# Kernel tuning notes

Hardware: AMD Instinct MI355X
Metric: run time of the kernel (lower is better)

## Reference

```python
import jax, jax.numpy as jnp
import numpy as np

WIN = 7
K1, K2 = 0.01, 0.03
NP_ = WIN * WIN
COV_NORM = NP_ / (NP_ - 1)


def _box_conv(x, w):
    return jax.lax.conv_general_dilated(
        x, w, window_strides=(1, 1), padding='VALID',
        dimension_numbers=('NCHW', 'OIHW', 'NCHW'))


def setup_inputs() -> dict:
    key = jax.random.key(0)
    k1, k2 = jax.random.split(key)
    B, C, H, W = 64, 2, 320, 320
    X = jax.random.uniform(k1, (B, C, H, W), dtype=jnp.float32)
    Y = jax.random.uniform(k2, (B, C, H, W), dtype=jnp.float32)
    data_range = jnp.ones((B, 1, 1, 1), dtype=jnp.float32)
    w = jnp.ones((1, C, WIN, WIN), dtype=jnp.float32) / (WIN * WIN)
    return {"X": X, "Y": Y, "data_range": data_range, "w": w}


def reference(X, Y, data_range, w):
    C1 = (K1 * data_range) ** 2
    C2 = (K2 * data_range) ** 2
    ux = _box_conv(X, w)
    uy = _box_conv(Y, w)
    uxx = _box_conv(X * X, w)
    uyy = _box_conv(Y * Y, w)
    uxy = _box_conv(X * Y, w)
    vx = COV_NORM * (uxx - ux * ux)
    vy = COV_NORM * (uyy - uy * uy)
    vxy = COV_NORM * (uxy - ux * uy)
    A1 = 2 * ux * uy + C1
    A2 = 2 * vxy + C2
    B1 = ux ** 2 + uy ** 2 + C1
    B2 = vx + vy + C2
    S = (A1 * A2) / (B1 * B2)
    return 1 - S.mean()
```

## Files before the change

### kernel.cpp

```cpp
#include <hip/hip_runtime.h>

#define WW 320
#define OWID 314
#define OHEI 314
#define BB 64
#define RPB 28
#define NBAND 12
#define NSTRIP 79
#define NTH 256
#define NBLK ((BB * NBAND * NSTRIP) / NTH)

__device__ __forceinline__ void compute_h(
    const float* __restrict__ X0, const float* __restrict__ X1,
    const float* __restrict__ Y0, const float* __restrict__ Y1,
    int off, int o2, float* __restrict__ h)
{
    float4 ax0 = *(const float4*)(X0 + off);
    float4 ax1 = *(const float4*)(X0 + off + 4);
    float4 ax2 = *(const float4*)(X0 + off + o2);
    float4 bx0 = *(const float4*)(X1 + off);
    float4 bx1 = *(const float4*)(X1 + off + 4);
    float4 bx2 = *(const float4*)(X1 + off + o2);
    float4 ay0 = *(const float4*)(Y0 + off);
    float4 ay1 = *(const float4*)(Y0 + off + 4);
    float4 ay2 = *(const float4*)(Y0 + off + o2);
    float4 by0 = *(const float4*)(Y1 + off);
    float4 by1 = *(const float4*)(Y1 + off + 4);
    float4 by2 = *(const float4*)(Y1 + off + o2);

    float x0[10] = {ax0.x, ax0.y, ax0.z, ax0.w, ax1.x, ax1.y, ax1.z, ax1.w, ax2.x, ax2.y};
    float x1[10] = {bx0.x, bx0.y, bx0.z, bx0.w, bx1.x, bx1.y, bx1.z, bx1.w, bx2.x, bx2.y};
    float y0[10] = {ay0.x, ay0.y, ay0.z, ay0.w, ay1.x, ay1.y, ay1.z, ay1.w, ay2.x, ay2.y};
    float y1[10] = {by0.x, by0.y, by0.z, by0.w, by1.x, by1.y, by1.z, by1.w, by2.x, by2.y};

    float sx[10], sy[10], sxx[10], syy[10], sxy[10];
    #pragma unroll
    for (int j = 0; j < 10; ++j) {
        sx[j]  = x0[j] + x1[j];
        sy[j]  = y0[j] + y1[j];
        sxx[j] = x0[j] * x0[j] + x1[j] * x1[j];
        syy[j] = y0[j] * y0[j] + y1[j] * y1[j];
        sxy[j] = x0[j] * y0[j] + x1[j] * y1[j];
    }
    #pragma unroll
    for (int q = 0; q < 5; ++q) {
        const float* m = (q == 0) ? sx : (q == 1) ? sy : (q == 2) ? sxx : (q == 3) ? syy : sxy;
        float t0 = ((m[0] + m[1]) + (m[2] + m[3])) + ((m[4] + m[5]) + m[6]);
        float t1 = t0 - m[0] + m[7];
        float t2 = t1 - m[1] + m[8];
        float t3 = t2 - m[2] + m[9];
        h[q * 4 + 0] = t0; h[q * 4 + 1] = t1; h[q * 4 + 2] = t2; h[q * 4 + 3] = t3;
    }
}

__global__ __launch_bounds__(NTH, 1) void ssim_main(
    const float* __restrict__ X, const float* __restrict__ Y,
    const float* __restrict__ dr, double* __restrict__ acc,
    unsigned* __restrict__ counter, float* __restrict__ out)
{
    const int wi   = blockIdx.x * NTH + threadIdx.x;
    const int s    = wi % NSTRIP;
    const int g    = wi / NSTRIP;
    const int band = g % NBAND;
    const int b    = g / NBAND;
    const int r0   = band * RPB;
    const int cb   = s * 4;
    const int o2   = (cb <= 308) ? 8 : 4;

    const size_t plane = (size_t)WW * WW;
    const float* X0 = X + (size_t)b * 2 * plane;
    const float* X1 = X0 + plane;
    const float* Y0 = Y + (size_t)b * 2 * plane;
    const float* Y1 = Y0 + plane;

    const float d  = dr[b];
    const float C1 = (0.01f * d) * (0.01f * d);
    const float C2 = (0.03f * d) * (0.03f * d);

    float cm[4];
    #pragma unroll
    for (int j = 0; j < 4; ++j) cm[j] = (cb + j < OWID) ? 1.0f : 0.0f;

    float ring[7][20];
    float v[20];
    #pragma unroll
    for (int i = 0; i < 20; ++i) v[i] = 0.0f;

    #pragma unroll
    for (int k = 0; k < 6; ++k) {
        compute_h(X0, X1, Y0, Y1, (r0 + k) * WW + cb, o2, &ring[k][0]);
        #pragma unroll
        for (int i = 0; i < 20; ++i) v[i] += ring[k][i];
    }

    float ssum = 0.0f;
    for (int t7 = 0; t7 < RPB; t7 += 7) {
        #pragma unroll
        for (int k = 0; k < 7; ++k) {
            const int t    = r0 + t7 + k;
            const int rin  = min(t + 6, WW - 1);
            const int slot = (k + 6) % 7;

            compute_h(X0, X1, Y0, Y1, rin * WW + cb, o2, &ring[slot][0]);
            #pragma unroll
            for (int i = 0; i < 20; ++i) v[i] += ring[slot][i];

            if (t < OHEI) {
                const float inv = 1.0f / 49.0f;
                const float cn  = 49.0f / 48.0f;
                #pragma unroll
                for (int j = 0; j < 4; ++j) {
                    float ux  = v[j]      * inv, uy  = v[4 + j]  * inv;
                    float uxx = v[8 + j]  * inv, uyy = v[12 + j] * inv, uxy = v[16 + j] * inv;
                    float vx  = cn * (uxx - ux * ux);
                    float vy  = cn * (uyy - uy * uy);
                    float vxy = cn * (uxy - ux * uy);
                    float A1  = 2.0f * ux * uy + C1;
                    float A2  = 2.0f * vxy + C2;
                    float B1  = ux * ux + uy * uy + C1;
                    float B2  = vx + vy + C2;
                    ssum += cm[j] * (A1 * A2) / (B1 * B2);
                }
            }

            #pragma unroll
            for (int i = 0; i < 20; ++i) v[i] -= ring[k][i];
        }
    }

    double local = (double)ssum;
    #pragma unroll
    for (int off = 32; off > 0; off >>= 1)
        local += __shfl_down(local, off, 64);
    __shared__ double wsum[NTH / 64];
    const int lane = threadIdx.x & 63, wid = threadIdx.x >> 6;
    if (lane == 0) wsum[wid] = local;
    __syncthreads();
    if (threadIdx.x == 0) {
        double tot = (wsum[0] + wsum[1]) + (wsum[2] + wsum[3]);
        atomicAdd(acc, tot);
        __threadfence();
        unsigned ticket = atomicAdd(counter, 1u);
        if (ticket == NBLK - 1) {
            double stot = atomicAdd(acc, 0.0);
            const double N = (double)BB * (double)OHEI * (double)OWID;
            out[0] = (float)(1.0 - stot / N);
        }
    }
}

extern "C" void kernel_launch(void* const* d_in, const int* in_sizes, int n_in,
                              void* d_out, int out_size, void* d_ws, size_t ws_size,
                              hipStream_t stream)
{
    const float* X  = (const float*)d_in[0];
    const float* Y  = (const float*)d_in[1];
    const float* dr = (const float*)d_in[2];
    double*   acc     = (double*)d_ws;
    unsigned* counter = (unsigned*)((char*)d_ws + 8);
    float*    out     = (float*)d_out;

    hipMemsetAsync(d_ws, 0, 16, stream);
    ssim_main<<<dim3(NBLK), dim3(NTH), 0, stream>>>(X, Y, dr, acc, counter, out);
}
```

Before: 153.5 us.

## Software-pipeline row loads one row ahead and shrink tail loads to float2

Splits the per-row work into a load phase and a math phase, so the loads for row i+1 are issued while the horizontal sums and SSIM terms for row i are computed. The prologue of six rows is folded into one unified 34-iteration loop, with the ring buffer zero-initialised and updated by delta. The third load per plane is narrowed from float4 to float2 because only two values are used. The extra register set for the prefetched row raises register pressure, and the loop now runs a few iterations longer with guard branches.

Measured after the change: 141.4 us. -7.9%, faster.

```diff
diff --git a/kernel.cpp b/kernel.cpp
--- a/kernel.cpp
+++ b/kernel.cpp
@@ -10,28 +10,31 @@
 #define NTH 256
 #define NBLK ((BB * NBAND * NSTRIP) / NTH)
 
-__device__ __forceinline__ void compute_h(
+__device__ __forceinline__ void load_row(
     const float* __restrict__ X0, const float* __restrict__ X1,
     const float* __restrict__ Y0, const float* __restrict__ Y1,
-    int off, int o2, float* __restrict__ h)
+    int off, int o2, float4 r4[8], float2 r2[4])
 {
-    float4 ax0 = *(const float4*)(X0 + off);
-    float4 ax1 = *(const float4*)(X0 + off + 4);
-    float4 ax2 = *(const float4*)(X0 + off + o2);
-    float4 bx0 = *(const float4*)(X1 + off);
-    float4 bx1 = *(const float4*)(X1 + off + 4);
-    float4 bx2 = *(const float4*)(X1 + off + o2);
-    float4 ay0 = *(const float4*)(Y0 + off);
-    float4 ay1 = *(const float4*)(Y0 + off + 4);
-    float4 ay2 = *(const float4*)(Y0 + off + o2);
-    float4 by0 = *(const float4*)(Y1 + off);
-    float4 by1 = *(const float4*)(Y1 + off + 4);
-    float4 by2 = *(const float4*)(Y1 + off + o2);
+    r4[0] = *(const float4*)(X0 + off);
+    r4[1] = *(const float4*)(X0 + off + 4);
+    r2[0] = *(const float2*)(X0 + off + o2);
+    r4[2] = *(const float4*)(X1 + off);
+    r4[3] = *(const float4*)(X1 + off + 4);
+    r2[1] = *(const float2*)(X1 + off + o2);
+    r4[4] = *(const float4*)(Y0 + off);
+    r4[5] = *(const float4*)(Y0 + off + 4);
+    r2[2] = *(const float2*)(Y0 + off + o2);
+    r4[6] = *(const float4*)(Y1 + off);
+    r4[7] = *(const float4*)(Y1 + off + 4);
+    r2[3] = *(const float2*)(Y1 + off + o2);
+}
 
-    float x0[10] = {ax0.x, ax0.y, ax0.z, ax0.w, ax1.x, ax1.y, ax1.z, ax1.w, ax2.x, ax2.y};
-    float x1[10] = {bx0.x, bx0.y, bx0.z, bx0.w, bx1.x, bx1.y, bx1.z, bx1.w, bx2.x, bx2.y};
-    float y0[10] = {ay0.x, ay0.y, ay0.z, ay0.w, ay1.x, ay1.y, ay1.z, ay1.w, ay2.x, ay2.y};
-    float y1[10] = {by0.x, by0.y, by0.z, by0.w, by1.x, by1.y, by1.z, by1.w, by2.x, by2.y};
+__device__ __forceinline__ void math_row(const float4 r4[8], const float2 r2[4], float h[20])
+{
+    float x0[10] = {r4[0].x, r4[0].y, r4[0].z, r4[0].w, r4[1].x, r4[1].y, r4[1].z, r4[1].w, r2[0].x, r2[0].y};
+    float x1[10] = {r4[2].x, r4[2].y, r4[2].z, r4[2].w, r4[3].x, r4[3].y, r4[3].z, r4[3].w, r2[1].x, r2[1].y};
+    float y0[10] = {r4[4].x, r4[4].y, r4[4].z, r4[4].w, r4[5].x, r4[5].y, r4[5].z, r4[5].w, r2[2].x, r2[2].y};
+    float y1[10] = {r4[6].x, r4[6].y, r4[6].z, r4[6].w, r4[7].x, r4[7].y, r4[7].z, r4[7].w, r2[3].x, r2[3].y};
 
     float sx[10], sy[10], sxx[10], syy[10], sxy[10];
     #pragma unroll
@@ -82,49 +85,63 @@
     for (int j = 0; j < 4; ++j) cm[j] = (cb + j < OWID) ? 1.0f : 0.0f;
 
     float ring[7][20];
+    #pragma unroll
+    for (int k = 0; k < 7; ++k)
+        #pragma unroll
+        for (int q = 0; q < 20; ++q) ring[k][q] = 0.0f;
+
     float v[20];
     #pragma unroll
-    for (int i = 0; i < 20; ++i) v[i] = 0.0f;
+    for (int q = 0; q < 20; ++q) v[q] = 0.0f;
 
-    #pragma unroll
-    for (int k = 0; k < 6; ++k) {
-        compute_h(X0, X1, Y0, Y1, (r0 + k) * WW + cb, o2, &ring[k][0]);
-        #pragma unroll
-        for (int i = 0; i < 20; ++i) v[i] += ring[k][i];
-    }
+    float4 c4[8], n4[8];
+    float2 c2[4], n2[4];
+    load_row(X0, X1, Y0, Y1, r0 * WW + cb, o2, c4, c2);
 
     float ssum = 0.0f;
-    for (int t7 = 0; t7 < RPB; t7 += 7) {
+    const float inv = 1.0f / 49.0f;
+    const float cn  = 49.0f / 48.0f;
+
+    for (int i7 = 0; i7 < 35; i7 += 7) {
         #pragma unroll
         for (int k = 0; k < 7; ++k) {
-            const int t    = r0 + t7 + k;
-            const int rin  = min(t + 6, WW - 1);
-            const int slot = (k + 6) % 7;
+            const int i = i7 + k;
 
-            compute_h(X0, X1, Y0, Y1, rin * WW + cb, o2, &ring[slot][0]);
-            #pragma unroll
-            for (int i = 0; i < 20; ++i) v[i] += ring[slot][i];
+            if (i < 33) {
+                const int rn = min(r0 + i + 1, WW - 1);
+                load_row(X0, X1, Y0, Y1, rn * WW + cb, o2, n4, n2);
+            }
+            if (i < 34) {
+                float h[20];
+                math_row(c4, c2, h);
+                #pragma unroll
+                for (int q = 0; q < 20; ++q) {
+                    v[q] += h[q] - ring[k][q];
+                    ring[k][q] = h[q];
+                }
 
-            if (t < OHEI) {
-                const float inv = 1.0f / 49.0f;
-                const float cn  = 49.0f / 48.0f;
+                const int t = r0 + i - 6;
+                if (i >= 6 && t < OHEI) {
+                    #pragma unroll
+                    for (int j = 0; j < 4; ++j) {
+                        float ux  = v[j]      * inv, uy  = v[4 + j]  * inv;
+                        float uxx = v[8 + j]  * inv, uyy = v[12 + j] * inv, uxy = v[16 + j] * inv;
+                        float vx  = cn * (uxx - ux * ux);
+                        float vy  = cn * (uyy - uy * uy);
+                        float vxy = cn * (uxy - ux * uy);
+                        float A1  = 2.0f * ux * uy + C1;
+                        float A2  = 2.0f * vxy + C2;
+                        float B1  = ux * ux + uy * uy + C1;
+                        float B2  = vx + vy + C2;
+                        ssum += cm[j] * (A1 * A2) / (B1 * B2);
+                    }
+                }
+
                 #pragma unroll
-                for (int j = 0; j < 4; ++j) {
-                    float ux  = v[j]      * inv, uy  = v[4 + j]  * inv;
-                    float uxx = v[8 + j]  * inv, uyy = v[12 + j] * inv, uxy = v[16 + j] * inv;
-                    float vx  = cn * (uxx - ux * ux);
-                    float vy  = cn * (uyy - uy * uy);
-                    float vxy = cn * (uxy - ux * uy);
-                    float A1  = 2.0f * ux * uy + C1;
-                    float A2  = 2.0f * vxy + C2;
-                    float B1  = ux * ux + uy * uy + C1;
-                    float B2  = vx + vy + C2;
-                    ssum += cm[j] * (A1 * A2) / (B1 * B2);
-                }
+                for (int q = 0; q < 8; ++q) c4[q] = n4[q];
+                #pragma unroll
+                for (int q = 0; q < 4; ++q) c2[q] = n2[q];
             }
-
-            #pragma unroll
-            for (int i = 0; i < 20; ++i) v[i] -= ring[k][i];
         }
     }
 
```

## Widen per-thread strip to six columns and double-buffer row loads

Applied to the files above, without the earlier changes.

Each thread now produces six output columns per row instead of four, and the band height drops from 28 to 20 rows across 16 bands. This lowers the horizontal halo overhead per output and reduces the number of overlapping loads. Row loads are software-pipelined with a two-slot register buffer so the next row's global reads are issued before the current row's math runs. The ring buffer is restructured into a single fully unrolled loop of 26 rows. The trade-off is much higher register pressure (a 7x30 ring, 30 running sums and 24 float4 buffers) and a larger vertical halo per band, since 6 halo rows are now shared by 20 outputs instead of 28.

After: 345.8 us. +125.3%, slower.

```diff
diff --git a/kernel.cpp b/kernel.cpp
--- a/kernel.cpp
+++ b/kernel.cpp
@@ -4,38 +4,43 @@
 #define OWID 314
 #define OHEI 314
 #define BB 64
-#define RPB 28
-#define NBAND 12
-#define NSTRIP 79
+#define SW 6
+#define NSTRIP 53
+#define RPB 20
+#define NBAND 16
+#define NROWS (RPB + 6)
 #define NTH 256
 #define NBLK ((BB * NBAND * NSTRIP) / NTH)
 
-__device__ __forceinline__ void compute_h(
+__device__ __forceinline__ void load_row(
     const float* __restrict__ X0, const float* __restrict__ X1,
     const float* __restrict__ Y0, const float* __restrict__ Y1,
-    int off, int o2, float* __restrict__ h)
+    int off, float4 r[12])
 {
-    float4 ax0 = *(const float4*)(X0 + off);
-    float4 ax1 = *(const float4*)(X0 + off + 4);
-    float4 ax2 = *(const float4*)(X0 + off + o2);
-    float4 bx0 = *(const float4*)(X1 + off);
-    float4 bx1 = *(const float4*)(X1 + off + 4);
-    float4 bx2 = *(const float4*)(X1 + off + o2);
-    float4 ay0 = *(const float4*)(Y0 + off);
-    float4 ay1 = *(const float4*)(Y0 + off + 4);
-    float4 ay2 = *(const float4*)(Y0 + off + o2);
-    float4 by0 = *(const float4*)(Y1 + off);
-    float4 by1 = *(const float4*)(Y1 + off + 4);
-    float4 by2 = *(const float4*)(Y1 + off + o2);
+    r[0]  = *(const float4*)(X0 + off);
+    r[1]  = *(const float4*)(X0 + off + 4);
+    r[2]  = *(const float4*)(X0 + off + 8);
+    r[3]  = *(const float4*)(X1 + off);
+    r[4]  = *(const float4*)(X1 + off + 4);
+    r[5]  = *(const float4*)(X1 + off + 8);
+    r[6]  = *(const float4*)(Y0 + off);
+    r[7]  = *(const float4*)(Y0 + off + 4);
+    r[8]  = *(const float4*)(Y0 + off + 8);
+    r[9]  = *(const float4*)(Y1 + off);
+    r[10] = *(const float4*)(Y1 + off + 4);
+    r[11] = *(const float4*)(Y1 + off + 8);
+}
 
-    float x0[10] = {ax0.x, ax0.y, ax0.z, ax0.w, ax1.x, ax1.y, ax1.z, ax1.w, ax2.x, ax2.y};
-    float x1[10] = {bx0.x, bx0.y, bx0.z, bx0.w, bx1.x, bx1.y, bx1.z, bx1.w, bx2.x, bx2.y};
-    float y0[10] = {ay0.x, ay0.y, ay0.z, ay0.w, ay1.x, ay1.y, ay1.z, ay1.w, ay2.x, ay2.y};
-    float y1[10] = {by0.x, by0.y, by0.z, by0.w, by1.x, by1.y, by1.z, by1.w, by2.x, by2.y};
+__device__ __forceinline__ void math_row(const float4 r[12], float h[30])
+{
+    float x0[12] = {r[0].x,r[0].y,r[0].z,r[0].w, r[1].x,r[1].y,r[1].z,r[1].w, r[2].x,r[2].y,r[2].z,r[2].w};
+    float x1[12] = {r[3].x,r[3].y,r[3].z,r[3].w, r[4].x,r[4].y,r[4].z,r[4].w, r[5].x,r[5].y,r[5].z,r[5].w};
+    float y0[12] = {r[6].x,r[6].y,r[6].z,r[6].w, r[7].x,r[7].y,r[7].z,r[7].w, r[8].x,r[8].y,r[8].z,r[8].w};
+    float y1[12] = {r[9].x,r[9].y,r[9].z,r[9].w, r[10].x,r[10].y,r[10].z,r[10].w, r[11].x,r[11].y,r[11].z,r[11].w};
 
-    float sx[10], sy[10], sxx[10], syy[10], sxy[10];
+    float sx[12], sy[12], sxx[12], syy[12], sxy[12];
     #pragma unroll
-    for (int j = 0; j < 10; ++j) {
+    for (int j = 0; j < 12; ++j) {
         sx[j]  = x0[j] + x1[j];
         sy[j]  = y0[j] + y1[j];
         sxx[j] = x0[j] * x0[j] + x1[j] * x1[j];
@@ -45,11 +50,13 @@
     #pragma unroll
     for (int q = 0; q < 5; ++q) {
         const float* m = (q == 0) ? sx : (q == 1) ? sy : (q == 2) ? sxx : (q == 3) ? syy : sxy;
-        float t0 = ((m[0] + m[1]) + (m[2] + m[3])) + ((m[4] + m[5]) + m[6]);
-        float t1 = t0 - m[0] + m[7];
-        float t2 = t1 - m[1] + m[8];
-        float t3 = t2 - m[2] + m[9];
-        h[q * 4 + 0] = t0; h[q * 4 + 1] = t1; h[q * 4 + 2] = t2; h[q * 4 + 3] = t3;
+        float t = ((m[0] + m[1]) + (m[2] + m[3])) + ((m[4] + m[5]) + m[6]);
+        h[q * 6 + 0] = t;
+        #pragma unroll
+        for (int j = 1; j < 6; ++j) {
+            t = t - m[j - 1] + m[j + 6];
+            h[q * 6 + j] = t;
+        }
     }
 }
 
@@ -64,8 +71,8 @@
     const int band = g % NBAND;
     const int b    = g / NBAND;
     const int r0   = band * RPB;
-    const int cb   = s * 4;
-    const int o2   = (cb <= 308) ? 8 : 4;
+    int cb = s * SW;
+    if (cb > WW - 12) cb = WW - 12;
 
     const size_t plane = (size_t)WW * WW;
     const float* X0 = X + (size_t)b * 2 * plane;
@@ -77,41 +84,51 @@
     const float C1 = (0.01f * d) * (0.01f * d);
     const float C2 = (0.03f * d) * (0.03f * d);
 
-    float cm[4];
+    float cm[SW];
     #pragma unroll
-    for (int j = 0; j < 4; ++j) cm[j] = (cb + j < OWID) ? 1.0f : 0.0f;
+    for (int j = 0; j < SW; ++j) cm[j] = (cb + j >= s * SW) ? 1.0f : 0.0f;
 
-    float ring[7][20];
-    float v[20];
+    float ring[7][30];
     #pragma unroll
-    for (int i = 0; i < 20; ++i) v[i] = 0.0f;
+    for (int k = 0; k < 7; ++k)
+        #pragma unroll
+        for (int q = 0; q < 30; ++q) ring[k][q] = 0.0f;
+
+    float v[30];
+    #pragma unroll
+    for (int q = 0; q < 30; ++q) v[q] = 0.0f;
+
+    float4 buf[2][12];
+    load_row(X0, X1, Y0, Y1, r0 * WW + cb, buf[0]);
+
+    float ssum = 0.0f;
+    const float inv = 1.0f / 49.0f;
+    const float cn  = 49.0f / 48.0f;
 
     #pragma unroll
-    for (int k = 0; k < 6; ++k) {
-        compute_h(X0, X1, Y0, Y1, (r0 + k) * WW + cb, o2, &ring[k][0]);
+    for (int i = 0; i < NROWS; ++i) {
+        if (i + 1 < NROWS) {
+            const int rn = min(r0 + i + 1, WW - 1);
+            load_row(X0, X1, Y0, Y1, rn * WW + cb, buf[(i + 1) & 1]);
+        }
+
+        float h[30];
+        math_row(buf[i & 1], h);
+
+        const int slot = i % 7;
         #pragma unroll
-        for (int i = 0; i < 20; ++i) v[i] += ring[k][i];
-    }
+        for (int q = 0; q < 30; ++q) {
+            v[q] += h[q] - ring[slot][q];
+            ring[slot][q] = h[q];
+        }
 
-    float ssum = 0.0f;
-    for (int t7 = 0; t7 < RPB; t7 += 7) {
-        #pragma unroll
-        for (int k = 0; k < 7; ++k) {
-            const int t    = r0 + t7 + k;
-            const int rin  = min(t + 6, WW - 1);
-            const int slot = (k + 6) % 7;
-
-            compute_h(X0, X1, Y0, Y1, rin * WW + cb, o2, &ring[slot][0]);
-            #pragma unroll
-            for (int i = 0; i < 20; ++i) v[i] += ring[slot][i];
-
+        if (i >= 6) {
+            const int t = r0 + i - 6;
             if (t < OHEI) {
-                const float inv = 1.0f / 49.0f;
-                const float cn  = 49.0f / 48.0f;
                 #pragma unroll
-                for (int j = 0; j < 4; ++j) {
-                    float ux  = v[j]      * inv, uy  = v[4 + j]  * inv;
-                    float uxx = v[8 + j]  * inv, uyy = v[12 + j] * inv, uxy = v[16 + j] * inv;
+                for (int j = 0; j < SW; ++j) {
+                    float ux  = v[j]       * inv, uy  = v[6 + j]  * inv;
+                    float uxx = v[12 + j]  * inv, uyy = v[18 + j] * inv, uxy = v[24 + j] * inv;
                     float vx  = cn * (uxx - ux * ux);
                     float vy  = cn * (uyy - uy * uy);
                     float vxy = cn * (uxy - ux * uy);
@@ -122,9 +139,6 @@
                     ssum += cm[j] * (A1 * A2) / (B1 * B2);
                 }
             }
-
-            #pragma unroll
-            for (int i = 0; i < 20; ++i) v[i] -= ring[k][i];
         }
     }
 
```
